# Performance work log

Hardware: AMD Instinct MI355X
Metric: run time of the kernel (lower is better)

The kernel has to match this reference:

```python
import jax, jax.numpy as jnp
import numpy as np

D = 1024
K = 256
B = 8192


def setup_inputs() -> dict:
    key = jax.random.key(0)
    kx, kw, kd, kp = jax.random.split(key, 4)
    x = jax.random.normal(kx, (B, D), dtype=jnp.float32)
    # scale weights ~1/sqrt(d) so the 11-matmul chain stays numerically sane
    Ws = jax.random.normal(kw, (10, D, D), dtype=jnp.float32) / jnp.sqrt(jnp.float32(D))
    W_dec = jax.random.normal(kd, (D, K), dtype=jnp.float32) / jnp.sqrt(jnp.float32(K))
    perm = jax.random.randint(kp, (K,), 0, D, dtype=jnp.int64)
    return {"x": x, "Ws": Ws, "W_dec": W_dec, "perm": perm}


def reference(x, Ws, W_dec, perm):
    # torch nn.Linear(d,d,bias=False): y = x @ W.T
    # source applies fc1..fc9, then fc9 AGAIN, then fc10 (11 matmuls, 10 weights)
    order = list(range(9)) + [8, 9]
    h = x
    for i in order:
        h = h @ Ws[i].T  # [B, D]
    y = h[:, perm]        # vectorized gather, replaces per-row python loop [B, K]
    out = y @ W_dec.T     # fc_decode: [B, D]
    return out
```

## Files before the change

kernel.cpp:

```cpp
#include <hip/hip_runtime.h>
#include <stdint.h>
#include <stddef.h>

typedef __bf16 bf16;
typedef __bf16 bf16x8 __attribute__((ext_vector_type(8)));
typedef float f32x4 __attribute__((ext_vector_type(4)));

__device__ __forceinline__ void global_to_lds16(const void* g, void* l) {
  const __attribute__((address_space(1))) unsigned* gp =
      reinterpret_cast<const __attribute__((address_space(1))) unsigned*>(
          reinterpret_cast<uintptr_t>(g));
  __attribute__((address_space(3))) unsigned* lp =
      reinterpret_cast<__attribute__((address_space(3))) unsigned*>(
          reinterpret_cast<uintptr_t>(l));
  __builtin_amdgcn_global_load_lds(gp, lp, 16, 0, 0);
}

template <typename OutT>
__device__ __forceinline__ void gemm128_body(const bf16* __restrict__ A,
                                             const bf16* __restrict__ B,
                                             OutT* __restrict__ C,
                                             int bx, int by) {
  __shared__ bf16 As[2][128 * 32];
  __shared__ bf16 Bs[2][128 * 32];

  const int tid = threadIdx.x;
  const int wave = tid >> 6, lane = tid & 63;
  const int quad = lane >> 4, l16 = lane & 15;
  const int rowBase = by * 128;
  const int colBase = bx * 128;
  const int waveM = (wave >> 1) * 64, waveN = (wave & 1) * 64;

  const int sr = tid >> 2;
  const int sc = (tid & 3) * 8;
  const bf16* Ag0 = A + (size_t)(rowBase + sr) * 1024 + sc;
  const bf16* Ag1 = Ag0 + (size_t)64 * 1024;
  const bf16* Bg0 = B + (size_t)(colBase + sr) * 1024 + sc;
  const bf16* Bg1 = Bg0 + (size_t)64 * 1024;

  char* lA0  = (char*)As[0] + wave * 1024;
  char* lA0b = lA0 + 4096;
  char* lA1  = (char*)As[1] + wave * 1024;
  char* lA1b = lA1 + 4096;
  char* lB0  = (char*)Bs[0] + wave * 1024;
  char* lB0b = lB0 + 4096;
  char* lB1  = (char*)Bs[1] + wave * 1024;
  char* lB1b = lB1 + 4096;

  f32x4 acc[4][4] = {};

  for (int k0 = 0; k0 < 1024; k0 += 64) {
    global_to_lds16(Ag0 + k0,      lA0);
    global_to_lds16(Ag1 + k0,      lA0b);
    global_to_lds16(Ag0 + k0 + 32, lA1);
    global_to_lds16(Ag1 + k0 + 32, lA1b);
    global_to_lds16(Bg0 + k0,      lB0);
    global_to_lds16(Bg1 + k0,      lB0b);
    global_to_lds16(Bg0 + k0 + 32, lB1);
    global_to_lds16(Bg1 + k0 + 32, lB1b);
    __syncthreads();
#pragma unroll
    for (int kk = 0; kk < 2; kk++) {
      bf16x8 af[4], bfr[4];
#pragma unroll
      for (int mi = 0; mi < 4; mi++)
        af[mi] = *(const bf16x8*)(As[kk] + (waveM + mi * 16 + l16) * 32 + quad * 8);
#pragma unroll
      for (int ni = 0; ni < 4; ni++)
        bfr[ni] = *(const bf16x8*)(Bs[kk] + (waveN + ni * 16 + l16) * 32 + quad * 8);
#pragma unroll
      for (int mi = 0; mi < 4; mi++)
#pragma unroll
        for (int ni = 0; ni < 4; ni++)
          acc[mi][ni] = __builtin_amdgcn_mfma_f32_16x16x32_bf16(af[mi], bfr[ni],
                                                                acc[mi][ni], 0, 0, 0);
    }
    __syncthreads();
  }

  OutT* Cb = C + (size_t)(rowBase + waveM) * 1024 + colBase + waveN;
#pragma unroll
  for (int mi = 0; mi < 4; mi++)
#pragma unroll
    for (int ni = 0; ni < 4; ni++)
#pragma unroll
      for (int r = 0; r < 4; r++)
        Cb[(size_t)(mi * 16 + quad * 4 + r) * 1024 + ni * 16 + l16] =
            (OutT)acc[mi][ni][r];
}

struct PrepArgs {
  const float* cvt_src[5]; bf16* cvt_dst[5];
  const float* tr_src[6];  bf16* tr_dst[6];
  const float* Wdec; const int* praw; bf16* Gbf;
};

__global__ __launch_bounds__(256) void prep_all(PrepArgs p) {
  __shared__ alignas(16) char smem[64 * 65 * 2];
  const int b = blockIdx.x;
  const int tid = threadIdx.x;

  if (b < 2560) {
    const int m = b >> 9, blk = b & 511;
    const float* __restrict__ src = p.cvt_src[m];
    bf16* __restrict__ dst = p.cvt_dst[m];
    const int i = (blk * 256 + tid) * 8;
    float4 a = *(const float4*)(src + i);
    float4 c = *(const float4*)(src + i + 4);
    bf16x8 o;
    o[0] = (bf16)a.x; o[1] = (bf16)a.y; o[2] = (bf16)a.z; o[3] = (bf16)a.w;
    o[4] = (bf16)c.x; o[5] = (bf16)c.y; o[6] = (bf16)c.z; o[7] = (bf16)c.w;
    *(bf16x8*)(dst + i) = o;
  } else if (b < 4096) {
    const int t = b - 2560;
    const int m = t >> 8, r = t & 255;
    const float* __restrict__ src = p.tr_src[m];
    bf16* __restrict__ dst = p.tr_dst[m];
    bf16(*tile)[65] = reinterpret_cast<bf16(*)[65]>(smem);
    const int bx = (r & 15) * 64;
    const int by = (r >> 4) * 64;
    const int tx = tid & 63;
    const int ty4 = tid >> 6;
#pragma unroll
    for (int rr = 0; rr < 16; rr++) {
      int row = ty4 * 16 + rr;
      tile[row][tx] = (bf16)src[(size_t)(by + row) * 1024 + bx + tx];
    }
    __syncthreads();
#pragma unroll
    for (int rr = 0; rr < 16; rr++) {
      int row = ty4 * 16 + rr;
      dst[(size_t)(bx + row) * 1024 + by + tx] = tile[tx][row];
    }
  } else {
    const int j = b - 4096;
    float* row = (float*)smem;
    int* perm_l = (int*)(smem + 4096);
    int* nzp = (int*)(smem + 4096 + 1024);
#pragma unroll
    for (int c = 0; c < 4; c++) row[tid * 4 + c] = 0.f;
    if (tid == 0) *nzp = 0;
    __syncthreads();
    if (tid < 128 && p.praw[2 * tid + 1] != 0) atomicOr(nzp, 1);
    __syncthreads();
    const int is64 = (*nzp == 0);
    perm_l[tid] = is64 ? p.praw[2 * tid] : p.praw[tid];
    __syncthreads();
    atomicAdd(&row[perm_l[tid]], p.Wdec[(size_t)j * 256 + tid]);
    __syncthreads();
#pragma unroll
    for (int c = 0; c < 4; c++)
      p.Gbf[(size_t)j * 1024 + tid * 4 + c] = (bf16)row[tid * 4 + c];
  }
}

struct TreeArgs {
  const bf16* A[6]; const bf16* B[6]; bf16* C[6];
  int nG;
  const float* x; bf16* xbf; int ubase;
};

__global__ __launch_bounds__(256) void tree_level(TreeArgs a) {
  const int b = blockIdx.x;
  const int gBlocks = a.nG * 64;
  if (b < gBlocks) {
    const int z = b >> 6, t = b & 63;
    gemm128_body<bf16>(a.A[z], a.B[z], a.C[z], t & 7, t >> 3);
  } else {
    const int unit = a.ubase + (b - gBlocks);
    const int i = unit * 2048 + (int)threadIdx.x * 8;
    float4 v0 = *(const float4*)(a.x + i);
    float4 v1 = *(const float4*)(a.x + i + 4);
    bf16x8 o;
    o[0] = (bf16)v0.x; o[1] = (bf16)v0.y; o[2] = (bf16)v0.z; o[3] = (bf16)v0.w;
    o[4] = (bf16)v1.x; o[5] = (bf16)v1.y; o[6] = (bf16)v1.z; o[7] = (bf16)v1.w;
    *(bf16x8*)(a.xbf + i) = o;
  }
}

__global__ __launch_bounds__(256) void final_gemm(const bf16* __restrict__ A,
                                                  const bf16* __restrict__ B,
                                                  float* __restrict__ C) {
  gemm128_body<float>(A, B, C, blockIdx.x, blockIdx.y);
}

extern "C" void kernel_launch(void* const* d_in, const int* in_sizes, int n_in,
                              void* d_out, int out_size, void* d_ws, size_t ws_size,
                              hipStream_t stream) {
  const float* x    = (const float*)d_in[0];
  const float* Wsrc = (const float*)d_in[1];
  const float* Wdec = (const float*)d_in[2];
  const int*   praw = (const int*)d_in[3];
  float* out = (float*)d_out;

  constexpr size_t MAT  = 1024ull * 1024ull;
  constexpr size_t SLOT = 2ull * 1024 * 1024;

  char* ws = (char*)d_ws;
  bf16* Wrm[5];
  for (int i = 0; i < 5; i++) Wrm[i] = (bf16*)(ws + (size_t)i * SLOT);
  bf16* Wt[6];
  for (int i = 0; i < 6; i++) Wt[i] = (bf16*)(ws + (size_t)(5 + i) * SLOT);
  bf16* Gbf = (bf16*)(ws + 11 * SLOT);
  bf16* xbf = (bf16*)(ws + 12 * SLOT);
  bf16* P[6];
  for (int i = 0; i < 6; i++) P[i] = (bf16*)(ws + (size_t)(20 + i) * SLOT);
  bf16* Q[3];
  for (int i = 0; i < 3; i++) Q[i] = (bf16*)(ws + (size_t)(26 + i) * SLOT);
  bf16* Rb = (bf16*)(ws + 29 * SLOT);
  bf16* Fb = (bf16*)(ws + 30 * SLOT);

  PrepArgs pa;
  const int rmIdx[5] = {1, 3, 5, 7, 8};
  for (int i = 0; i < 5; i++) { pa.cvt_src[i] = Wsrc + (size_t)rmIdx[i] * MAT; pa.cvt_dst[i] = Wrm[i]; }
  const int trIdx[6] = {0, 2, 4, 6, 8, 9};
  for (int i = 0; i < 6; i++) { pa.tr_src[i] = Wsrc + (size_t)trIdx[i] * MAT; pa.tr_dst[i] = Wt[i]; }
  pa.Wdec = Wdec; pa.praw = praw; pa.Gbf = Gbf;
  prep_all<<<dim3(5120), 256, 0, stream>>>(pa);

  TreeArgs L1{};
  const bf16* l1a[6] = {Gbf, Wt[4], Wrm[3], Wt[2], Wrm[1], Wt[0]};
  const bf16* l1b[6] = {Wt[5], Wrm[4], Wt[3], Wrm[2], Wt[1], Wrm[0]};
  for (int i = 0; i < 6; i++) { L1.A[i] = l1a[i]; L1.B[i] = l1b[i]; L1.C[i] = P[i]; }
  L1.nG = 6; L1.x = x; L1.xbf = xbf; L1.ubase = 0;
  tree_level<<<dim3(384), 256, 0, stream>>>(L1);

  TreeArgs L2{};
  const bf16* l2a[3] = {P[0], P[3], P[5]};
  const bf16* l2b[3] = {P[1], P[2], P[4]};
  for (int i = 0; i < 3; i++) { L2.A[i] = l2a[i]; L2.B[i] = l2b[i]; L2.C[i] = Q[i]; }
  L2.nG = 3; L2.x = x; L2.xbf = xbf; L2.ubase = 0;
  tree_level<<<dim3(192 + 1360), 256, 0, stream>>>(L2);

  TreeArgs L3{};
  L3.A[0] = Q[0]; L3.B[0] = Q[1]; L3.C[0] = Rb;
  L3.nG = 1; L3.x = x; L3.xbf = xbf; L3.ubase = 1360;
  tree_level<<<dim3(64 + 1360), 256, 0, stream>>>(L3);

  TreeArgs L4{};
  L4.A[0] = Rb; L4.B[0] = Q[2]; L4.C[0] = Fb;
  L4.nG = 1; L4.x = x; L4.xbf = xbf; L4.ubase = 2720;
  tree_level<<<dim3(64 + 1376), 256, 0, stream>>>(L4);

  final_gemm<<<dim3(8, 64), 256, 0, stream>>>(xbf, Fb, out);

  (void)in_sizes; (void)n_in; (void)out_size; (void)ws_size;
}
```

Baseline: 218.0 us.

## Fuse prep and GEMM tree levels into one cooperative persistent kernel

Replaces the separate prep, four tree-level and final GEMM launches with a single cooperative kernel of at most 512 blocks. Blocks loop over each phase's work units and meet at grid-wide barriers. The x-to-bf16 conversion moves into the prep phase; before, it filled idle CUs during the narrow tree levels. The aim is to cut kernel launch and inter-kernel gaps, at the cost of grid-sync latency and losing that overlap, with a multi-launch fallback if the cooperative launch fails.

```diff
diff --git a/kernel.cpp b/kernel.cpp
--- a/kernel.cpp
+++ b/kernel.cpp
@@ -1,6 +1,9 @@
 #include <hip/hip_runtime.h>
+#include <hip/hip_cooperative_groups.h>
 #include <stdint.h>
 #include <stddef.h>
+
+namespace cg = cooperative_groups;
 
 typedef __bf16 bf16;
 typedef __bf16 bf16x8 __attribute__((ext_vector_type(8)));
@@ -17,12 +20,13 @@
 }
 
 template <typename OutT>
-__device__ __forceinline__ void gemm128_body(const bf16* __restrict__ A,
+__device__ __forceinline__ void gemm128_body(char* smem,
+                                             const bf16* __restrict__ A,
                                              const bf16* __restrict__ B,
                                              OutT* __restrict__ C,
                                              int bx, int by) {
-  __shared__ bf16 As[2][128 * 32];
-  __shared__ bf16 Bs[2][128 * 32];
+  bf16* Asl[2] = {(bf16*)smem, (bf16*)(smem + 8192)};
+  bf16* Bsl[2] = {(bf16*)(smem + 16384), (bf16*)(smem + 24576)};
 
   const int tid = threadIdx.x;
   const int wave = tid >> 6, lane = tid & 63;
@@ -38,13 +42,13 @@
   const bf16* Bg0 = B + (size_t)(colBase + sr) * 1024 + sc;
   const bf16* Bg1 = Bg0 + (size_t)64 * 1024;
 
-  char* lA0  = (char*)As[0] + wave * 1024;
+  char* lA0  = (char*)Asl[0] + wave * 1024;
   char* lA0b = lA0 + 4096;
-  char* lA1  = (char*)As[1] + wave * 1024;
+  char* lA1  = (char*)Asl[1] + wave * 1024;
   char* lA1b = lA1 + 4096;
-  char* lB0  = (char*)Bs[0] + wave * 1024;
+  char* lB0  = (char*)Bsl[0] + wave * 1024;
   char* lB0b = lB0 + 4096;
-  char* lB1  = (char*)Bs[1] + wave * 1024;
+  char* lB1  = (char*)Bsl[1] + wave * 1024;
   char* lB1b = lB1 + 4096;
 
   f32x4 acc[4][4] = {};
@@ -64,10 +68,10 @@
       bf16x8 af[4], bfr[4];
 #pragma unroll
       for (int mi = 0; mi < 4; mi++)
-        af[mi] = *(const bf16x8*)(As[kk] + (waveM + mi * 16 + l16) * 32 + quad * 8);
+        af[mi] = *(const bf16x8*)(Asl[kk] + (waveM + mi * 16 + l16) * 32 + quad * 8);
 #pragma unroll
       for (int ni = 0; ni < 4; ni++)
-        bfr[ni] = *(const bf16x8*)(Bs[kk] + (waveN + ni * 16 + l16) * 32 + quad * 8);
+        bfr[ni] = *(const bf16x8*)(Bsl[kk] + (waveN + ni * 16 + l16) * 32 + quad * 8);
 #pragma unroll
       for (int mi = 0; mi < 4; mi++)
 #pragma unroll
@@ -89,19 +93,22 @@
             (OutT)acc[mi][ni][r];
 }
 
-struct PrepArgs {
+struct AllArgs {
   const float* cvt_src[5]; bf16* cvt_dst[5];
   const float* tr_src[6];  bf16* tr_dst[6];
   const float* Wdec; const int* praw; bf16* Gbf;
+  const float* x; bf16* xbf;
+  const bf16* A1[6]; const bf16* B1[6]; bf16* C1[6];
+  const bf16* A2[3]; const bf16* B2[3]; bf16* C2[3];
+  const bf16* A3; const bf16* B3; bf16* C3;
+  const bf16* A4; const bf16* B4; bf16* C4;
+  const bf16* Af; const bf16* Bf; float* Cf;
 };
 
-__global__ __launch_bounds__(256) void prep_all(PrepArgs p) {
-  __shared__ alignas(16) char smem[64 * 65 * 2];
-  const int b = blockIdx.x;
+__device__ __forceinline__ void prep_unit(const AllArgs& p, int u, char* smem) {
   const int tid = threadIdx.x;
-
-  if (b < 2560) {
-    const int m = b >> 9, blk = b & 511;
+  if (u < 2560) {
+    const int m = u >> 9, blk = u & 511;
     const float* __restrict__ src = p.cvt_src[m];
     bf16* __restrict__ dst = p.cvt_dst[m];
     const int i = (blk * 256 + tid) * 8;
@@ -111,8 +118,8 @@
     o[0] = (bf16)a.x; o[1] = (bf16)a.y; o[2] = (bf16)a.z; o[3] = (bf16)a.w;
     o[4] = (bf16)c.x; o[5] = (bf16)c.y; o[6] = (bf16)c.z; o[7] = (bf16)c.w;
     *(bf16x8*)(dst + i) = o;
-  } else if (b < 4096) {
-    const int t = b - 2560;
+  } else if (u < 4096) {
+    const int t = u - 2560;
     const int m = t >> 8, r = t & 255;
     const float* __restrict__ src = p.tr_src[m];
     bf16* __restrict__ dst = p.tr_dst[m];
@@ -132,8 +139,8 @@
       int row = ty4 * 16 + rr;
       dst[(size_t)(bx + row) * 1024 + by + tx] = tile[tx][row];
     }
-  } else {
-    const int j = b - 4096;
+  } else if (u < 5120) {
+    const int j = u - 4096;
     float* row = (float*)smem;
     int* perm_l = (int*)(smem + 4096);
     int* nzp = (int*)(smem + 4096 + 1024);
@@ -151,37 +158,81 @@
 #pragma unroll
     for (int c = 0; c < 4; c++)
       p.Gbf[(size_t)j * 1024 + tid * 4 + c] = (bf16)row[tid * 4 + c];
-  }
-}
-
-struct TreeArgs {
-  const bf16* A[6]; const bf16* B[6]; bf16* C[6];
-  int nG;
-  const float* x; bf16* xbf; int ubase;
-};
-
-__global__ __launch_bounds__(256) void tree_level(TreeArgs a) {
-  const int b = blockIdx.x;
-  const int gBlocks = a.nG * 64;
-  if (b < gBlocks) {
-    const int z = b >> 6, t = b & 63;
-    gemm128_body<bf16>(a.A[z], a.B[z], a.C[z], t & 7, t >> 3);
   } else {
-    const int unit = a.ubase + (b - gBlocks);
-    const int i = unit * 2048 + (int)threadIdx.x * 8;
-    float4 v0 = *(const float4*)(a.x + i);
-    float4 v1 = *(const float4*)(a.x + i + 4);
+    const int i = (u - 5120) * 2048 + tid * 8;
+    float4 v0 = *(const float4*)(p.x + i);
+    float4 v1 = *(const float4*)(p.x + i + 4);
     bf16x8 o;
     o[0] = (bf16)v0.x; o[1] = (bf16)v0.y; o[2] = (bf16)v0.z; o[3] = (bf16)v0.w;
     o[4] = (bf16)v1.x; o[5] = (bf16)v1.y; o[6] = (bf16)v1.z; o[7] = (bf16)v1.w;
-    *(bf16x8*)(a.xbf + i) = o;
-  }
-}
-
-__global__ __launch_bounds__(256) void final_gemm(const bf16* __restrict__ A,
-                                                  const bf16* __restrict__ B,
-                                                  float* __restrict__ C) {
-  gemm128_body<float>(A, B, C, blockIdx.x, blockIdx.y);
+    *(bf16x8*)(p.xbf + i) = o;
+  }
+}
+
+__global__ __launch_bounds__(256) void mega(AllArgs a) {
+  __shared__ alignas(16) char smem[32768];
+  cg::grid_group grid = cg::this_grid();
+  const int b = blockIdx.x;
+  const int G = gridDim.x;
+
+#pragma unroll 1
+  for (int u = b; u < 9216; u += G) { prep_unit(a, u, smem); __syncthreads(); }
+  grid.sync();
+
+#pragma unroll 1
+  for (int t = b; t < 384; t += G) {
+    const int z = t >> 6, tt = t & 63;
+    gemm128_body<bf16>(smem, a.A1[z], a.B1[z], a.C1[z], tt & 7, tt >> 3);
+  }
+  grid.sync();
+
+#pragma unroll 1
+  for (int t = b; t < 192; t += G) {
+    const int z = t >> 6, tt = t & 63;
+    gemm128_body<bf16>(smem, a.A2[z], a.B2[z], a.C2[z], tt & 7, tt >> 3);
+  }
+  grid.sync();
+
+#pragma unroll 1
+  for (int t = b; t < 64; t += G)
+    gemm128_body<bf16>(smem, a.A3, a.B3, a.C3, t & 7, t >> 3);
+  grid.sync();
+
+#pragma unroll 1
+  for (int t = b; t < 64; t += G)
+    gemm128_body<bf16>(smem, a.A4, a.B4, a.C4, t & 7, t >> 3);
+  grid.sync();
+
+#pragma unroll 1
+  for (int t = b; t < 512; t += G)
+    gemm128_body<float>(smem, a.Af, a.Bf, a.Cf, t & 7, t >> 3);
+}
+
+__global__ __launch_bounds__(256) void fb_prep(AllArgs a) {
+  __shared__ alignas(16) char smem[32768];
+  prep_unit(a, blockIdx.x, smem);
+}
+__global__ __launch_bounds__(256) void fb_l1(AllArgs a) {
+  __shared__ alignas(16) char smem[32768];
+  const int t = blockIdx.x, z = t >> 6, tt = t & 63;
+  gemm128_body<bf16>(smem, a.A1[z], a.B1[z], a.C1[z], tt & 7, tt >> 3);
+}
+__global__ __launch_bounds__(256) void fb_l2(AllArgs a) {
+  __shared__ alignas(16) char smem[32768];
+  const int t = blockIdx.x, z = t >> 6, tt = t & 63;
+  gemm128_body<bf16>(smem, a.A2[z], a.B2[z], a.C2[z], tt & 7, tt >> 3);
+}
+__global__ __launch_bounds__(256) void fb_l3(AllArgs a) {
+  __shared__ alignas(16) char smem[32768];
+  gemm128_body<bf16>(smem, a.A3, a.B3, a.C3, blockIdx.x & 7, blockIdx.x >> 3);
+}
+__global__ __launch_bounds__(256) void fb_l4(AllArgs a) {
+  __shared__ alignas(16) char smem[32768];
+  gemm128_body<bf16>(smem, a.A4, a.B4, a.C4, blockIdx.x & 7, blockIdx.x >> 3);
+}
+__global__ __launch_bounds__(256) void fb_final(AllArgs a) {
+  __shared__ alignas(16) char smem[32768];
+  gemm128_body<float>(smem, a.Af, a.Bf, a.Cf, blockIdx.x & 7, blockIdx.x >> 3);
 }
 
 extern "C" void kernel_launch(void* const* d_in, const int* in_sizes, int n_in,
@@ -210,39 +261,44 @@
   bf16* Rb = (bf16*)(ws + 29 * SLOT);
   bf16* Fb = (bf16*)(ws + 30 * SLOT);
 
-  PrepArgs pa;
+  AllArgs aa{};
   const int rmIdx[5] = {1, 3, 5, 7, 8};
-  for (int i = 0; i < 5; i++) { pa.cvt_src[i] = Wsrc + (size_t)rmIdx[i] * MAT; pa.cvt_dst[i] = Wrm[i]; }
+  for (int i = 0; i < 5; i++) { aa.cvt_src[i] = Wsrc + (size_t)rmIdx[i] * MAT; aa.cvt_dst[i] = Wrm[i]; }
   const int trIdx[6] = {0, 2, 4, 6, 8, 9};
-  for (int i = 0; i < 6; i++) { pa.tr_src[i] = Wsrc + (size_t)trIdx[i] * MAT; pa.tr_dst[i] = Wt[i]; }
-  pa.Wdec = Wdec; pa.praw = praw; pa.Gbf = Gbf;
-  prep_all<<<dim3(5120), 256, 0, stream>>>(pa);
-
-  TreeArgs L1{};
+  for (int i = 0; i < 6; i++) { aa.tr_src[i] = Wsrc + (size_t)trIdx[i] * MAT; aa.tr_dst[i] = Wt[i]; }
+  aa.Wdec = Wdec; aa.praw = praw; aa.Gbf = Gbf;
+  aa.x = x; aa.xbf = xbf;
+
   const bf16* l1a[6] = {Gbf, Wt[4], Wrm[3], Wt[2], Wrm[1], Wt[0]};
   const bf16* l1b[6] = {Wt[5], Wrm[4], Wt[3], Wrm[2], Wt[1], Wrm[0]};
-  for (int i = 0; i < 6; i++) { L1.A[i] = l1a[i]; L1.B[i] = l1b[i]; L1.C[i] = P[i]; }
-  L1.nG = 6; L1.x = x; L1.xbf = xbf; L1.ubase = 0;
-  tree_level<<<dim3(384), 256, 0, stream>>>(L1);
-
-  TreeArgs L2{};
+  for (int i = 0; i < 6; i++) { aa.A1[i] = l1a[i]; aa.B1[i] = l1b[i]; aa.C1[i] = P[i]; }
   const bf16* l2a[3] = {P[0], P[3], P[5]};
   const bf16* l2b[3] = {P[1], P[2], P[4]};
-  for (int i = 0; i < 3; i++) { L2.A[i] = l2a[i]; L2.B[i] = l2b[i]; L2.C[i] = Q[i]; }
-  L2.nG = 3; L2.x = x; L2.xbf = xbf; L2.ubase = 0;
-  tree_level<<<dim3(192 + 1360), 256, 0, stream>>>(L2);
-
-  TreeArgs L3{};
-  L3.A[0] = Q[0]; L3.B[0] = Q[1]; L3.C[0] = Rb;
-  L3.nG = 1; L3.x = x; L3.xbf = xbf; L3.ubase = 1360;
-  tree_level<<<dim3(64 + 1360), 256, 0, stream>>>(L3);
-
-  TreeArgs L4{};
-  L4.A[0] = Rb; L4.B[0] = Q[2]; L4.C[0] = Fb;
-  L4.nG = 1; L4.x = x; L4.xbf = xbf; L4.ubase = 2720;
-  tree_level<<<dim3(64 + 1376), 256, 0, stream>>>(L4);
-
-  final_gemm<<<dim3(8, 64), 256, 0, stream>>>(xbf, Fb, out);
+  for (int i = 0; i < 3; i++) { aa.A2[i] = l2a[i]; aa.B2[i] = l2b[i]; aa.C2[i] = Q[i]; }
+  aa.A3 = Q[0]; aa.B3 = Q[1]; aa.C3 = Rb;
+  aa.A4 = Rb;   aa.B4 = Q[2]; aa.C4 = Fb;
+  aa.Af = xbf;  aa.Bf = Fb;   aa.Cf = out;
+
+  bool coop_done = false;
+  int nbPerCU = 0;
+  hipError_t qe = hipOccupancyMaxActiveBlocksPerMultiprocessor(&nbPerCU, mega, 256, 0);
+  if (qe == hipSuccess && nbPerCU >= 1) {
+    int G = nbPerCU * 256;
+    if (G > 512) G = 512;
+    void* args[] = {(void*)&aa};
+    hipError_t le = hipLaunchCooperativeKernel((const void*)mega, dim3(G),
+                                               dim3(256), args, 0, stream);
+    coop_done = (le == hipSuccess);
+  }
+
+  if (!coop_done) {
+    fb_prep <<<dim3(9216), 256, 0, stream>>>(aa);
+    fb_l1   <<<dim3(384),  256, 0, stream>>>(aa);
+    fb_l2   <<<dim3(192),  256, 0, stream>>>(aa);
+    fb_l3   <<<dim3(64),   256, 0, stream>>>(aa);
+    fb_l4   <<<dim3(64),   256, 0, stream>>>(aa);
+    fb_final<<<dim3(512),  256, 0, stream>>>(aa);
+  }
 
   (void)in_sizes; (void)n_in; (void)out_size; (void)ws_size;
 }
```

New measurement: 222.8 us. 2.2% more time.
